# Kernel optimization log

Hardware: AMD Instinct MI355X
Metric: run time of the kernel (lower is better)

The kernel has to match this reference:

```python
import jax, jax.numpy as jnp
import numpy as np

H = 2048        # hidden_size
NH = 16         # num query heads
NKV = 4         # num kv heads
HD = 128        # head_dim
EPS = 1e-6
SCALE = HD ** -0.5
GROUPS = NH // NKV


def rotate_half(x):
    x1, x2 = x[..., : HD // 2], x[..., HD // 2:]
    return jnp.concatenate((-x2, x1), axis=-1)


def rmsnorm(x, w):
    # x: [..., HD]
    var = jnp.mean(jnp.square(x), axis=-1, keepdims=True)
    return x * jax.lax.rsqrt(var + EPS) * w


def setup_inputs() -> dict:
    key = jax.random.key(0)
    ks = jax.random.split(key, 10)
    B, QL, CL = 4, 1024, 3072
    s = 0.02
    return {
        "noise": jax.random.normal(ks[0], (B, QL, H), jnp.float32),
        "ctx": jax.random.normal(ks[1], (B, CL, H), jnp.float32),
        "cos": jax.random.uniform(ks[2], (B, CL + QL, HD), jnp.float32, -1.0, 1.0),
        "sin": jax.random.uniform(ks[3], (B, CL + QL, HD), jnp.float32, -1.0, 1.0),
        "Wq": jax.random.normal(ks[4], (H, NH * HD), jnp.float32) * s,
        "Wk": jax.random.normal(ks[5], (H, NKV * HD), jnp.float32) * s,
        "Wv": jax.random.normal(ks[6], (H, NKV * HD), jnp.float32) * s,
        "Wo": jax.random.normal(ks[7], (NH * HD, H), jnp.float32) * s,
        "qn_w": jnp.ones((HD,), jnp.float32),
        "kn_w": jnp.ones((HD,), jnp.float32),
    }


def reference(noise, ctx, cos, sin, Wq, Wk, Wv, Wo, qn_w, kn_w):
    B, QL, _ = noise.shape
    CL = ctx.shape[1]
    KL = CL + QL

    # Q from noise
    q = (noise @ Wq).reshape(B, QL, NH, HD)
    q = rmsnorm(q, qn_w).transpose(0, 2, 1, 3)            # [B, NH, QL, HD]

    # K/V from [ctx ; noise]
    kv_in = jnp.concatenate([ctx, noise], axis=1)          # [B, KL, H]
    k = (kv_in @ Wk).reshape(B, KL, NKV, HD)
    k = rmsnorm(k, kn_w).transpose(0, 2, 1, 3)             # [B, NKV, KL, HD]
    v = (kv_in @ Wv).reshape(B, KL, NKV, HD).transpose(0, 2, 1, 3)

    # RoPE: queries use last QL positions
    cos_q, sin_q = cos[:, -QL:, None].transpose(0, 2, 1, 3), sin[:, -QL:, None].transpose(0, 2, 1, 3)
    cos_k, sin_k = cos[:, None], sin[:, None]
    q = q * cos_q + rotate_half(q) * sin_q
    k = k * cos_k + rotate_half(k) * sin_k

    # GQA expansion
    k = jnp.repeat(k, GROUPS, axis=1)                      # [B, NH, KL, HD]
    v = jnp.repeat(v, GROUPS, axis=1)

    attn = jnp.einsum('bhqd,bhkd->bhqk', q, k) * SCALE     # [B, NH, QL, KL]
    attn = jax.nn.softmax(attn.astype(jnp.float32), axis=-1).astype(v.dtype)
    out = jnp.einsum('bhqk,bhkd->bhqd', attn, v)
    out = out.transpose(0, 2, 1, 3).reshape(B, QL, NH * HD)
    return out @ Wo
```

## Files before the change

kernel.cpp:

```cpp
#include <hip/hip_runtime.h>
#include <cstdint>
#include <cstddef>

#define DEVI __device__ __forceinline__

typedef short bf16x8 __attribute__((ext_vector_type(8)));
typedef short bf16x4 __attribute__((ext_vector_type(4)));
typedef float f32x4  __attribute__((ext_vector_type(4)));

constexpr int H_  = 2048;
constexpr int NH  = 16;
constexpr int NKV = 4;
constexpr int HD  = 128;
constexpr int B_  = 4;
constexpr int QL  = 1024;
constexpr int CL  = 3072;
constexpr int KL  = 4096;
constexpr float EPS = 1e-6f;
constexpr float SCALE_LOG2E = 0.08838834764831845f * 1.4426950408889634f;

DEVI unsigned short f2bf(float x) {
  unsigned int u = __float_as_uint(x);
  u += 0x7FFFu + ((u >> 16) & 1u);
  return (unsigned short)(u >> 16);
}
DEVI float bf2f(unsigned short u) {
  return __uint_as_float(((unsigned int)u) << 16);
}
DEVI bf16x4 mk4(float a, float b, float c, float d) {
  unsigned ua = __float_as_uint(a) + 0x8000u, ub = __float_as_uint(b) + 0x8000u;
  unsigned uc = __float_as_uint(c) + 0x8000u, ud = __float_as_uint(d) + 0x8000u;
  union { unsigned u[2]; bf16x4 v; } r;
  r.u[0] = __builtin_amdgcn_perm(ub, ua, 0x07060302u);
  r.u[1] = __builtin_amdgcn_perm(ud, uc, 0x07060302u);
  return r.v;
}

DEVI void async16(const void* g, void* l) {
  __builtin_amdgcn_global_load_lds(
      (const __attribute__((address_space(1))) void*)g,
      (__attribute__((address_space(3))) void*)l, 16, 0, 0);
}

__global__ __launch_bounds__(256)
void prep(const float* __restrict__ noise, const float* __restrict__ ctx,
          unsigned short* __restrict__ kvin) {
  const size_t t = (size_t)blockIdx.x * 256 + threadIdx.x;
  const size_t e = t * 8;
  const int row = (int)(e / H_), col = (int)(e % H_);
  const int b = row >> 12, pos = row & 4095;
  const float* src = (pos < CL) ? ctx + ((size_t)(b * CL + pos)) * H_ + col
                                : noise + ((size_t)(b * QL + (pos - CL))) * H_ + col;
  float4 x = ((const float4*)src)[0], y = ((const float4*)src)[1];
  bf16x8 v;
  v[0] = (short)f2bf(x.x); v[1] = (short)f2bf(x.y);
  v[2] = (short)f2bf(x.z); v[3] = (short)f2bf(x.w);
  v[4] = (short)f2bf(y.x); v[5] = (short)f2bf(y.y);
  v[6] = (short)f2bf(y.z); v[7] = (short)f2bf(y.w);
  *(bf16x8*)(kvin + e) = v;
}

__global__ __launch_bounds__(256)
void wtrans(const float* __restrict__ in, unsigned short* __restrict__ out,
            int K, int N) {
  __shared__ float t[64][65];
  const int ktiles = K >> 6;
  const int kt = blockIdx.x % ktiles;
  const int nt = blockIdx.x / ktiles;
  {
    const int r = threadIdx.x >> 2, cs = threadIdx.x & 3;
    const float4* src = (const float4*)(in + (size_t)(kt * 64 + r) * N + nt * 64 + cs * 16);
    #pragma unroll
    for (int i = 0; i < 4; ++i) {
      float4 v = src[i];
      t[r][cs * 16 + i * 4 + 0] = v.x;
      t[r][cs * 16 + i * 4 + 1] = v.y;
      t[r][cs * 16 + i * 4 + 2] = v.z;
      t[r][cs * 16 + i * 4 + 3] = v.w;
    }
  }
  __syncthreads();
  {
    const int n = threadIdx.x >> 2, ks = threadIdx.x & 3;
    bf16x8 o0, o1;
    #pragma unroll
    for (int i = 0; i < 8; ++i) o0[i] = (short)f2bf(t[ks * 16 + i][n]);
    #pragma unroll
    for (int i = 0; i < 8; ++i) o1[i] = (short)f2bf(t[ks * 16 + 8 + i][n]);
    unsigned short* op = out + (size_t)(nt * 64 + n) * K + kt * 64 + ks * 16;
    *(bf16x8*)(op) = o0;
    *(bf16x8*)(op + 8) = o1;
  }
}

template <int MODE>
__global__ __launch_bounds__(256)
void gemm2(const unsigned short* __restrict__ Abf,
           const unsigned short* __restrict__ Bt,
           const float* __restrict__ normw,
           const float* __restrict__ cosb, const float* __restrict__ sinb,
           unsigned short* __restrict__ outb, float* __restrict__ outf) {
  constexpr int M  = (MODE == 1 || MODE == 2) ? (B_ * KL) : (B_ * QL);
  constexpr int K  = H_;
  constexpr int MT = M / 128;

  __shared__ union U {
    struct { unsigned short a[128][64]; unsigned short b[128][64]; } st;
    unsigned short ct[128][138];
  } sm;

  const int tid  = threadIdx.x;
  const int tm   = blockIdx.x % MT;
  const int tn   = blockIdx.x / MT;
  const int wid  = tid >> 6, lane = tid & 63, quad = lane >> 4, lm = lane & 15;
  const int wm   = wid >> 1, wn = wid & 1;

  f32x4 acc[4][4];
  #pragma unroll
  for (int i = 0; i < 4; ++i)
    #pragma unroll
    for (int j = 0; j < 4; ++j)
      #pragma unroll
      for (int r = 0; r < 4; ++r) acc[i][j][r] = 0.f;

  const unsigned short* agp[4];
  const unsigned short* bgp[4];
  #pragma unroll
  for (int i = 0; i < 4; ++i) {
    const int idx = i * 256 + tid;
    const int arow = idx >> 3, g = idx & 7, gg = g ^ (arow & 7);
    int grow;
    if constexpr (MODE == 0) {
      const int gmr = tm * 128 + arow;
      grow = (gmr >> 10) * KL + CL + (gmr & 1023);
    } else {
      grow = tm * 128 + arow;
    }
    agp[i] = Abf + (size_t)grow * K + gg * 8;
    bgp[i] = Bt + (size_t)(tn * 128 + arow) * K + gg * 8;
  }

  for (int kt = 0; kt < K / 64; ++kt) {
    __syncthreads();
    #pragma unroll
    for (int i = 0; i < 4; ++i) {
      async16(agp[i] + kt * 64, (char*)&sm.st.a[0][0] + (i * 256 + wid * 64) * 16);
      async16(bgp[i] + kt * 64, (char*)&sm.st.b[0][0] + (i * 256 + wid * 64) * 16);
    }
    __syncthreads();
    #pragma unroll
    for (int ks = 0; ks < 2; ++ks) {
      bf16x8 af[4], bfr[4];
      #pragma unroll
      for (int i = 0; i < 4; ++i) {
        const int swz = (ks * 4 + quad) ^ (lm & 7);
        af[i] = *(const bf16x8*)&sm.st.a[wm * 64 + i * 16 + lm][swz * 8];
      }
      #pragma unroll
      for (int j = 0; j < 4; ++j) {
        const int swz = (ks * 4 + quad) ^ (lm & 7);
        bfr[j] = *(const bf16x8*)&sm.st.b[wn * 64 + j * 16 + lm][swz * 8];
      }
      #pragma unroll
      for (int i = 0; i < 4; ++i)
        #pragma unroll
        for (int j = 0; j < 4; ++j)
          acc[i][j] = __builtin_amdgcn_mfma_f32_16x16x32_bf16(af[i], bfr[j], acc[i][j], 0, 0, 0);
    }
  }

  if constexpr (MODE == 3) {
    #pragma unroll
    for (int i = 0; i < 4; ++i)
      #pragma unroll
      for (int j = 0; j < 4; ++j) {
        const int row = tm * 128 + wm * 64 + i * 16 + quad * 4;
        const int col = tn * 128 + wn * 64 + j * 16 + lm;
        #pragma unroll
        for (int rr = 0; rr < 4; ++rr)
          outf[(size_t)(row + rr) * H_ + col] = acc[i][j][rr];
      }
    return;
  }

  __syncthreads();
  #pragma unroll
  for (int i = 0; i < 4; ++i)
    #pragma unroll
    for (int j = 0; j < 4; ++j)
      #pragma unroll
      for (int rr = 0; rr < 4; ++rr)
        sm.ct[wm * 64 + i * 16 + quad * 4 + rr][wn * 64 + j * 16 + lm] =
            f2bf(acc[i][j][rr]);
  __syncthreads();

  const int row2 = tid >> 1, half = tid & 1;
  if constexpr (MODE == 0 || MODE == 1) {
    const int gmr = tm * 128 + row2;
    int ci; size_t obase;
    if constexpr (MODE == 0) {
      const int b = gmr >> 10, pos = gmr & 1023;
      ci = (b * KL + CL + pos) * HD;
      obase = ((size_t)((b * NH + tn) * QL + pos)) * HD;
    } else {
      const int b = gmr >> 12, pos = gmr & 4095;
      ci = (b * KL + pos) * HD;
      obase = ((size_t)((b * NKV + tn) * KL + pos)) * HD;
    }
    float ss = 0.f;
    for (int d = half * 64; d < half * 64 + 64; ++d) {
      float v = bf2f(sm.ct[row2][d]);
      ss += v * v;
    }
    ss += __shfl_xor(ss, 1);
    const float rinv = rsqrtf(ss * (1.0f / 128.0f) + EPS);
    constexpr float OSC = (MODE == 0) ? SCALE_LOG2E : 1.0f;
    #pragma unroll
    for (int d8 = 0; d8 < 8; ++d8) {
      bf16x8 v;
      #pragma unroll
      for (int j = 0; j < 8; ++j) {
        const int d = half * 64 + d8 * 8 + j;
        const float x  = bf2f(sm.ct[row2][d])      * rinv * normw[d];
        const float xo = bf2f(sm.ct[row2][d ^ 64]) * rinv * normw[d ^ 64];
        const float rot = (d < 64) ? -xo : xo;
        v[j] = (short)f2bf((x * cosb[ci + d] + rot * sinb[ci + d]) * OSC);
      }
      *(bf16x8*)(outb + obase + half * 64 + d8 * 8) = v;
    }
  } else {
    const int d = row2;
    const int b = (tm * 128) >> 12;
    const int posBase = ((tm * 128) & 4095) + half * 64;
    const size_t obase = ((size_t)((b * NKV + tn) * HD + d)) * KL + posBase;
    #pragma unroll
    for (int k8 = 0; k8 < 8; ++k8) {
      bf16x8 v;
      #pragma unroll
      for (int j = 0; j < 8; ++j)
        v[j] = (short)sm.ct[half * 64 + k8 * 8 + j][d];
      *(bf16x8*)(outb + obase + k8 * 8) = v;
    }
  }
}

__global__ __launch_bounds__(256)
void attn2(const unsigned short* __restrict__ qb,
           const unsigned short* __restrict__ kb,
           const unsigned short* __restrict__ vtb,
           unsigned short* __restrict__ ao) {
  __shared__ unsigned short kl[64][128];
  __shared__ unsigned short vl[128][64];

  const int tid = threadIdx.x;
  const int wave = tid >> 6, lane = tid & 63, quad = lane >> 4, lm = lane & 15;
  const int qblk = blockIdx.x & 7;
  const int bh = blockIdx.x >> 3;
  const int b = bh >> 4, h = bh & 15, kvh = h >> 2;
  const int q0 = qblk * 128 + wave * 32;

  bf16x8 qf[2][4];
  const unsigned short* qbase = qb + ((size_t)((b * NH + h) * QL + q0)) * HD;
  #pragma unroll
  for (int qt = 0; qt < 2; ++qt)
    #pragma unroll
    for (int kq = 0; kq < 4; ++kq)
      qf[qt][kq] = *(const bf16x8*)(qbase + (qt * 16 + lm) * HD + kq * 32 + quad * 8);

  f32x4 o[2][8];
  float li[2] = {0.f, 0.f};
  #pragma unroll
  for (int qt = 0; qt < 2; ++qt)
    #pragma unroll
    for (int dt = 0; dt < 8; ++dt)
      #pragma unroll
      for (int rr = 0; rr < 4; ++rr) o[qt][dt][rr] = 0.f;

  const unsigned short* kbase = kb + ((size_t)(b * NKV + kvh)) * KL * HD;
  const unsigned short* vbase = vtb + ((size_t)(b * NKV + kvh)) * HD * KL;

  const unsigned short* kgp[4];
  const unsigned short* vgp[4];
  #pragma unroll
  for (int i = 0; i < 4; ++i) {
    const int idx = i * 256 + tid;
    const int krow = idx >> 4, gc = idx & 15;
    const int gg = (gc & 8) | ((gc & 7) ^ (krow & 7));
    kgp[i] = kbase + (size_t)krow * HD + gg * 8;
    const int vrow = idx >> 3, g = idx & 7;
    const int gv = g ^ (vrow & 7);
    vgp[i] = vbase + (size_t)vrow * KL + gv * 8;
  }

  for (int kt = 0; kt < KL / 64; ++kt) {
    __syncthreads();
    #pragma unroll
    for (int i = 0; i < 4; ++i) {
      async16(kgp[i] + (size_t)kt * 64 * HD, (char*)&kl[0][0] + (i * 256 + wave * 64) * 16);
      async16(vgp[i] + kt * 64,              (char*)&vl[0][0] + (i * 256 + wave * 64) * 16);
    }
    __syncthreads();

    #pragma unroll
    for (int nt = 0; nt < 4; ++nt) {
      bf16x8 kf[4];
      #pragma unroll
      for (int kq = 0; kq < 4; ++kq) {
        const int gc = kq * 4 + quad;
        const int swz = (gc & 8) | ((gc & 7) ^ (lm & 7));
        kf[kq] = *(const bf16x8*)&kl[nt * 16 + lm][swz * 8];
      }
      f32x4 s0 = {0.f, 0.f, 0.f, 0.f}, s1 = {0.f, 0.f, 0.f, 0.f};
      #pragma unroll
      for (int kq = 0; kq < 4; ++kq) {
        s0 = __builtin_amdgcn_mfma_f32_16x16x32_bf16(kf[kq], qf[0][kq], s0, 0, 0, 0);
        s1 = __builtin_amdgcn_mfma_f32_16x16x32_bf16(kf[kq], qf[1][kq], s1, 0, 0, 0);
      }
      float e00 = __builtin_amdgcn_exp2f(s0[0]), e01 = __builtin_amdgcn_exp2f(s0[1]);
      float e02 = __builtin_amdgcn_exp2f(s0[2]), e03 = __builtin_amdgcn_exp2f(s0[3]);
      float e10 = __builtin_amdgcn_exp2f(s1[0]), e11 = __builtin_amdgcn_exp2f(s1[1]);
      float e12 = __builtin_amdgcn_exp2f(s1[2]), e13 = __builtin_amdgcn_exp2f(s1[3]);
      li[0] += (e00 + e01) + (e02 + e03);
      li[1] += (e10 + e11) + (e12 + e13);
      bf16x4 p0 = mk4(e00, e01, e02, e03);
      bf16x4 p1 = mk4(e10, e11, e12, e13);
      #pragma unroll
      for (int dt = 0; dt < 8; ++dt) {
        const int gv = (nt * 2 + (quad >> 1)) ^ (lm & 7);
        bf16x4 vf = *(const bf16x4*)&vl[dt * 16 + lm][gv * 8 + (quad & 1) * 4];
        o[0][dt] = __builtin_amdgcn_mfma_f32_16x16x16bf16_1k(vf, p0, o[0][dt], 0, 0, 0);
        o[1][dt] = __builtin_amdgcn_mfma_f32_16x16x16bf16_1k(vf, p1, o[1][dt], 0, 0, 0);
      }
    }
  }

  #pragma unroll
  for (int qt = 0; qt < 2; ++qt) {
    float l = li[qt];
    l += __shfl_xor(l, 16);
    l += __shfl_xor(l, 32);
    const float inv = 1.0f / l;
    const size_t rowbase = ((size_t)(b * QL + q0 + qt * 16 + lm)) * (NH * HD) + h * HD;
    #pragma unroll
    for (int dt = 0; dt < 8; ++dt) {
      bf16x4 v = mk4(o[qt][dt][0] * inv, o[qt][dt][1] * inv,
                     o[qt][dt][2] * inv, o[qt][dt][3] * inv);
      *(bf16x4*)(ao + rowbase + dt * 16 + quad * 4) = v;
    }
  }
}

extern "C" void kernel_launch(void* const* d_in, const int* in_sizes, int n_in,
                              void* d_out, int out_size, void* d_ws, size_t ws_size,
                              hipStream_t stream) {
  const float* noise = (const float*)d_in[0];
  const float* ctx   = (const float*)d_in[1];
  const float* cosb  = (const float*)d_in[2];
  const float* sinb  = (const float*)d_in[3];
  const float* Wq    = (const float*)d_in[4];
  const float* Wk    = (const float*)d_in[5];
  const float* Wv    = (const float*)d_in[6];
  const float* Wo    = (const float*)d_in[7];
  const float* qn    = (const float*)d_in[8];
  const float* kn    = (const float*)d_in[9];
  float* out = (float*)d_out;

  char* ws = (char*)d_ws;
  unsigned short* kvin = (unsigned short*)(ws);
  unsigned short* aob  = (unsigned short*)(ws);
  unsigned short* WqT  = (unsigned short*)(ws + 67108864);
  unsigned short* WkT  = (unsigned short*)(ws + 67108864 + 8388608);
  unsigned short* WvT  = (unsigned short*)(ws + 67108864 + 10485760);
  unsigned short* WoT  = (unsigned short*)(ws + 67108864 + 12582912);
  unsigned short* qbuf = (unsigned short*)(ws + 67108864 + 20971520);
  unsigned short* kbuf = (unsigned short*)(ws + 67108864 + 37748736);
  unsigned short* vtb  = (unsigned short*)(ws + 67108864 + 54525952);

  prep<<<dim3((B_ * KL * H_) / 8 / 256), dim3(256), 0, stream>>>(noise, ctx, kvin);

  wtrans<<<dim3(1024), dim3(256), 0, stream>>>(Wq, WqT, 2048, 2048);
  wtrans<<<dim3(256),  dim3(256), 0, stream>>>(Wk, WkT, 2048, 512);
  wtrans<<<dim3(256),  dim3(256), 0, stream>>>(Wv, WvT, 2048, 512);
  wtrans<<<dim3(1024), dim3(256), 0, stream>>>(Wo, WoT, 2048, 2048);

  gemm2<0><<<dim3(32 * 16), dim3(256), 0, stream>>>(
      kvin, WqT, qn, cosb, sinb, qbuf, nullptr);
  gemm2<1><<<dim3(128 * 4), dim3(256), 0, stream>>>(
      kvin, WkT, kn, cosb, sinb, kbuf, nullptr);
  gemm2<2><<<dim3(128 * 4), dim3(256), 0, stream>>>(
      kvin, WvT, nullptr, nullptr, nullptr, vtb, nullptr);

  attn2<<<dim3(512), dim3(256), 0, stream>>>(qbuf, kbuf, vtb, aob);

  gemm2<3><<<dim3(32 * 16), dim3(256), 0, stream>>>(
      aob, WoT, nullptr, nullptr, nullptr, nullptr, out);
}
```

Baseline: 599.4 us.

## Halve attention query tile per wave, double grid, add MFMA priority hints

Each attention wave now handles 16 query rows instead of 32, so a block covers 64 queries and the grid grows from 512 to 1024 blocks. Register pressure drops, and launch bounds now ask for 4 blocks per CU, to improve occupancy and spread work over the 256 CUs. s_setprio hints are placed around the MFMA sections. The cost is that each K/V tile loaded into LDS is reused by half as many queries, which doubles global K/V traffic and the LDS reads per MFMA.

```diff
diff --git a/kernel.cpp b/kernel.cpp
--- a/kernel.cpp
+++ b/kernel.cpp
@@ -244,7 +244,7 @@
   }
 }
 
-__global__ __launch_bounds__(256)
+__global__ __launch_bounds__(256, 4)
 void attn2(const unsigned short* __restrict__ qb,
            const unsigned short* __restrict__ kb,
            const unsigned short* __restrict__ vtb,
@@ -254,27 +254,23 @@
 
   const int tid = threadIdx.x;
   const int wave = tid >> 6, lane = tid & 63, quad = lane >> 4, lm = lane & 15;
-  const int qblk = blockIdx.x & 7;
-  const int bh = blockIdx.x >> 3;
+  const int qblk = blockIdx.x & 15;
+  const int bh = blockIdx.x >> 4;
   const int b = bh >> 4, h = bh & 15, kvh = h >> 2;
-  const int q0 = qblk * 128 + wave * 32;
-
-  bf16x8 qf[2][4];
+  const int q0 = qblk * 64 + wave * 16;
+
+  bf16x8 qf[4];
   const unsigned short* qbase = qb + ((size_t)((b * NH + h) * QL + q0)) * HD;
   #pragma unroll
-  for (int qt = 0; qt < 2; ++qt)
-    #pragma unroll
-    for (int kq = 0; kq < 4; ++kq)
-      qf[qt][kq] = *(const bf16x8*)(qbase + (qt * 16 + lm) * HD + kq * 32 + quad * 8);
-
-  f32x4 o[2][8];
-  float li[2] = {0.f, 0.f};
-  #pragma unroll
-  for (int qt = 0; qt < 2; ++qt)
-    #pragma unroll
-    for (int dt = 0; dt < 8; ++dt)
-      #pragma unroll
-      for (int rr = 0; rr < 4; ++rr) o[qt][dt][rr] = 0.f;
+  for (int kq = 0; kq < 4; ++kq)
+    qf[kq] = *(const bf16x8*)(qbase + lm * HD + kq * 32 + quad * 8);
+
+  f32x4 o[8];
+  float li = 0.f;
+  #pragma unroll
+  for (int dt = 0; dt < 8; ++dt)
+    #pragma unroll
+    for (int rr = 0; rr < 4; ++rr) o[dt][rr] = 0.f;
 
   const unsigned short* kbase = kb + ((size_t)(b * NKV + kvh)) * KL * HD;
   const unsigned short* vbase = vtb + ((size_t)(b * NKV + kvh)) * HD * KL;
@@ -310,41 +306,37 @@
         const int swz = (gc & 8) | ((gc & 7) ^ (lm & 7));
         kf[kq] = *(const bf16x8*)&kl[nt * 16 + lm][swz * 8];
       }
-      f32x4 s0 = {0.f, 0.f, 0.f, 0.f}, s1 = {0.f, 0.f, 0.f, 0.f};
-      #pragma unroll
-      for (int kq = 0; kq < 4; ++kq) {
-        s0 = __builtin_amdgcn_mfma_f32_16x16x32_bf16(kf[kq], qf[0][kq], s0, 0, 0, 0);
-        s1 = __builtin_amdgcn_mfma_f32_16x16x32_bf16(kf[kq], qf[1][kq], s1, 0, 0, 0);
-      }
+      f32x4 s0 = {0.f, 0.f, 0.f, 0.f};
+      __builtin_amdgcn_s_setprio(1);
+      #pragma unroll
+      for (int kq = 0; kq < 4; ++kq)
+        s0 = __builtin_amdgcn_mfma_f32_16x16x32_bf16(kf[kq], qf[kq], s0, 0, 0, 0);
+      __builtin_amdgcn_s_setprio(0);
       float e00 = __builtin_amdgcn_exp2f(s0[0]), e01 = __builtin_amdgcn_exp2f(s0[1]);
       float e02 = __builtin_amdgcn_exp2f(s0[2]), e03 = __builtin_amdgcn_exp2f(s0[3]);
-      float e10 = __builtin_amdgcn_exp2f(s1[0]), e11 = __builtin_amdgcn_exp2f(s1[1]);
-      float e12 = __builtin_amdgcn_exp2f(s1[2]), e13 = __builtin_amdgcn_exp2f(s1[3]);
-      li[0] += (e00 + e01) + (e02 + e03);
-      li[1] += (e10 + e11) + (e12 + e13);
+      li += (e00 + e01) + (e02 + e03);
       bf16x4 p0 = mk4(e00, e01, e02, e03);
-      bf16x4 p1 = mk4(e10, e11, e12, e13);
+      __builtin_amdgcn_s_setprio(1);
       #pragma unroll
       for (int dt = 0; dt < 8; ++dt) {
         const int gv = (nt * 2 + (quad >> 1)) ^ (lm & 7);
         bf16x4 vf = *(const bf16x4*)&vl[dt * 16 + lm][gv * 8 + (quad & 1) * 4];
-        o[0][dt] = __builtin_amdgcn_mfma_f32_16x16x16bf16_1k(vf, p0, o[0][dt], 0, 0, 0);
-        o[1][dt] = __builtin_amdgcn_mfma_f32_16x16x16bf16_1k(vf, p1, o[1][dt], 0, 0, 0);
-      }
-    }
-  }
-
-  #pragma unroll
-  for (int qt = 0; qt < 2; ++qt) {
-    float l = li[qt];
+        o[dt] = __builtin_amdgcn_mfma_f32_16x16x16bf16_1k(vf, p0, o[dt], 0, 0, 0);
+      }
+      __builtin_amdgcn_s_setprio(0);
+    }
+  }
+
+  {
+    float l = li;
     l += __shfl_xor(l, 16);
     l += __shfl_xor(l, 32);
     const float inv = 1.0f / l;
-    const size_t rowbase = ((size_t)(b * QL + q0 + qt * 16 + lm)) * (NH * HD) + h * HD;
+    const size_t rowbase = ((size_t)(b * QL + q0 + lm)) * (NH * HD) + h * HD;
     #pragma unroll
     for (int dt = 0; dt < 8; ++dt) {
-      bf16x4 v = mk4(o[qt][dt][0] * inv, o[qt][dt][1] * inv,
-                     o[qt][dt][2] * inv, o[qt][dt][3] * inv);
+      bf16x4 v = mk4(o[dt][0] * inv, o[dt][1] * inv,
+                     o[dt][2] * inv, o[dt][3] * inv);
       *(bf16x4*)(ao + rowbase + dt * 16 + quad * 4) = v;
     }
   }
@@ -390,7 +382,7 @@
   gemm2<2><<<dim3(128 * 4), dim3(256), 0, stream>>>(
       kvin, WvT, nullptr, nullptr, nullptr, vtb, nullptr);
 
-  attn2<<<dim3(512), dim3(256), 0, stream>>>(qbuf, kbuf, vtb, aob);
+  attn2<<<dim3(1024), dim3(256), 0, stream>>>(qbuf, kbuf, vtb, aob);
 
   gemm2<3><<<dim3(32 * 16), dim3(256), 0, stream>>>(
       aob, WoT, nullptr, nullptr, nullptr, nullptr, out);
```

Measured after the change: 638.2 us. 1.06x slower.
